# Performance work log

Hardware: AMD Instinct MI355X
Metric: run time of the kernel (lower is better)

Reference implementation:

```python
import jax, jax.numpy as jnp
import numpy as np

DIM = 512
N_HEADS = 8
HEAD_DIM = DIM // N_HEADS


def setup_inputs() -> dict:
    key = jax.random.key(0)
    ks = jax.random.split(key, 11)
    B, S = 2, 2048
    s = 1.0 / np.sqrt(DIM)
    return {
        "q": jax.random.normal(ks[0], (B, S, DIM), jnp.float32),
        "k": jax.random.normal(ks[1], (B, S, DIM), jnp.float32),
        "v": jax.random.normal(ks[2], (B, S, DIM), jnp.float32),
        "Wq": jax.random.normal(ks[3], (DIM, DIM), jnp.float32) * s,
        "bq": jnp.zeros((DIM,), jnp.float32),
        "Wk": jax.random.normal(ks[4], (DIM, DIM), jnp.float32) * s,
        "bk": jnp.zeros((DIM,), jnp.float32),
        "Wv": jax.random.normal(ks[5], (DIM, DIM), jnp.float32) * s,
        "bv": jnp.zeros((DIM,), jnp.float32),
        "Wo": jax.random.normal(ks[6], (DIM, DIM), jnp.float32) * s,
        "bo": jnp.zeros((DIM,), jnp.float32),
    }


def reference(q, k, v, Wq, bq, Wk, bk, Wv, bv, Wo, bo):
    B, S, _ = q.shape
    # projections; split into heads: [B, H, S, Dh]
    def proj(x, W, b):
        y = x @ W.T + b
        return y.reshape(B, -1, N_HEADS, HEAD_DIM).transpose(0, 2, 1, 3)

    qh = proj(q, Wq, bq)
    kh = proj(k, Wk, bk)
    vh = proj(v, Wv, bv)
    scores = jnp.einsum("bhsd,bhtd->bhst", qh, kh) / np.sqrt(HEAD_DIM)
    attn = jax.nn.softmax(scores, axis=-1)  # dropout = identity in eval
    ctx = jnp.einsum("bhst,bhtd->bhsd", attn, vh)
    ctx = ctx.transpose(0, 2, 1, 3).reshape(B, S, DIM)
    out = ctx @ Wo.T + bo
    return out, attn
```

## Files before the change

### kernel.cpp

```cpp
#include <hip/hip_runtime.h>
#include <math.h>

#define DIM 512
#define NH 8
#define HD 64
#define SS 2048
#define NB 2

typedef __bf16 bf16;
typedef __attribute__((ext_vector_type(8))) __bf16 bf16x8;
typedef __attribute__((ext_vector_type(4))) __bf16 bf16x4;
typedef __attribute__((ext_vector_type(2))) __bf16 bf16x2;
typedef __attribute__((ext_vector_type(4))) float f32x4;

__device__ inline bf16x8 cvt8(const float* s) {
  bf16x8 o;
#pragma unroll
  for (int i = 0; i < 8; ++i) o[i] = (bf16)s[i];
  return o;
}

__device__ inline void bar_lds_only() {
  asm volatile("s_waitcnt lgkmcnt(0)" ::: "memory");
  __builtin_amdgcn_s_barrier();
}

__global__ __launch_bounds__(256) void qkv_proj_kernel(
    const float* __restrict__ xq, const float* __restrict__ xk, const float* __restrict__ xv,
    const float* __restrict__ Wq, const float* __restrict__ bq,
    const float* __restrict__ Wk, const float* __restrict__ bk,
    const float* __restrict__ Wv, const float* __restrict__ bv,
    bf16* __restrict__ qh, bf16* __restrict__ kh, bf16* __restrict__ vh)
{
  const int which = blockIdx.z;
  const float* A    = (which == 0) ? xq : (which == 1) ? xk : xv;
  const float* W    = (which == 0) ? Wq : (which == 1) ? Wk : Wv;
  const float* bias = (which == 0) ? bq : (which == 1) ? bk : bv;
  bf16* out         = (which == 0) ? qh : (which == 1) ? kh : vh;
  const float oscale = (which == 0) ? 0.125f : 1.0f;

  __shared__ bf16 As[128][72];
  __shared__ bf16 Bs[64][72];

  const int m0 = blockIdx.x * 128;
  const int n0 = blockIdx.y * 64;
  const int tid = threadIdx.x;
  const int w = tid >> 6, l = tid & 63;
  const int l16 = l & 15, lg = l >> 4;
  const int wm = w >> 1, wn = w & 1;

  f32x4 acc[4][2];
#pragma unroll
  for (int mf = 0; mf < 4; ++mf)
#pragma unroll
    for (int nf = 0; nf < 2; ++nf) acc[mf][nf] = (f32x4){0.f, 0.f, 0.f, 0.f};

  for (int k0 = 0; k0 < DIM; k0 += 64) {
    __syncthreads();
    {
      const int r = tid >> 1, hf = (tid & 1) * 32;
      const float* src = &A[(size_t)(m0 + r) * DIM + k0 + hf];
      bf16* dst = &As[r][hf];
#pragma unroll
      for (int i = 0; i < 4; ++i) ((bf16x8*)dst)[i] = cvt8(src + i * 8);
    }
    if (tid < 128) {
      const int r = tid >> 1, hf = (tid & 1) * 32;
      const float* src = &W[(size_t)(n0 + r) * DIM + k0 + hf];
      bf16* dst = &Bs[r][hf];
#pragma unroll
      for (int i = 0; i < 4; ++i) ((bf16x8*)dst)[i] = cvt8(src + i * 8);
    }
    __syncthreads();

#pragma unroll
    for (int kk = 0; kk < 2; ++kk) {
      bf16x8 bfr[2];
      bfr[0] = *(const bf16x8*)&Bs[wn * 32 + l16][kk * 32 + lg * 8];
      bfr[1] = *(const bf16x8*)&Bs[wn * 32 + 16 + l16][kk * 32 + lg * 8];
#pragma unroll
      for (int mf = 0; mf < 4; ++mf) {
        const bf16x8 af = *(const bf16x8*)&As[wm * 64 + mf * 16 + l16][kk * 32 + lg * 8];
        acc[mf][0] = __builtin_amdgcn_mfma_f32_16x16x32_bf16(af, bfr[0], acc[mf][0], 0, 0, 0);
        acc[mf][1] = __builtin_amdgcn_mfma_f32_16x16x32_bf16(af, bfr[1], acc[mf][1], 0, 0, 0);
      }
    }
  }

  const int h = blockIdx.y;
#pragma unroll
  for (int mf = 0; mf < 4; ++mf) {
#pragma unroll
    for (int nf = 0; nf < 2; ++nf) {
      const int d = wn * 32 + nf * 16 + l16;
#pragma unroll
      for (int ri = 0; ri < 4; ++ri) {
        const int row = m0 + wm * 64 + mf * 16 + lg * 4 + ri;
        const int b = row >> 11, s = row & 2047;
        out[((size_t)(b * NH + h) * SS + s) * HD + d] =
            (bf16)((acc[mf][nf][ri] + bias[n0 + d]) * oscale);
      }
    }
  }
}

__global__ __launch_bounds__(512, 4) void attn_kernel(
    const bf16* __restrict__ qh, const bf16* __restrict__ kh, const bf16* __restrict__ vh,
    float* __restrict__ attn, bf16* __restrict__ ctx)
{
  __shared__ __align__(16) bf16 Ks[2][64][72];
  __shared__ __align__(16) bf16 Vt[2][64][72];
  __shared__ __align__(16) bf16 Ps[8][16][128];
  __shared__ float mlred[2][4][16];

  const int lin  = blockIdx.x;
  const int work = (lin & 7) * 64 + (lin >> 3);
  const int bh = work >> 5;
  const int q0 = (work & 31) * 64;

  const int tid = threadIdx.x;
  const int w   = tid >> 6;
  const int wq  = w >> 1;
  const int wt  = w & 1;
  const int l   = tid & 63;
  const int l16 = l & 15;
  const int lg  = l >> 4;

  const bf16* qp = qh + (size_t)bh * SS * HD;
  const bf16* kp = kh + (size_t)bh * SS * HD;
  const bf16* vp = vh + (size_t)bh * SS * HD;

  const int ks_wt = tid >> 8;
  const int ks_r  = (tid >> 2) & 63;
  const int ks_c  = (tid & 3) * 16;
  const int vs_wt = tid >> 8;
  const int vs_rc = (tid >> 3) & 31;
  const int vs_dc = tid & 7;

  const bf16* kstage = &kp[(size_t)(ks_wt * 1024 + ks_r) * HD + ks_c];
  const bf16* vstage = &vp[(size_t)(vs_wt * 1024 + vs_rc * 2) * HD + vs_dc * 8];
  bf16* ks_dst = &Ks[ks_wt][ks_r][ks_c];
  const int vcolbase = (((vs_rc >> 2) ^ vs_dc) << 3) | ((vs_rc & 3) << 1);

  const int qrow = q0 + wq * 16 + l16;
  const bf16x8 qf0 = *(const bf16x8*)&qp[(size_t)qrow * HD + lg * 8];
  const bf16x8 qf1 = *(const bf16x8*)&qp[(size_t)qrow * HD + 32 + lg * 8];

  const int tbase = wt * 1024;

  float lsum = 0.f;
  {
    const bf16* src = kstage;
    ((bf16x8*)ks_dst)[0] = ((const bf16x8*)src)[0];
    ((bf16x8*)ks_dst)[1] = ((const bf16x8*)src)[1];
  }
  for (int tt = 0; tt < 1024; tt += 64) {
    bf16x8 kr0, kr1;
    const bool has_next = (tt + 64) < 1024;
    if (has_next) {
      const bf16* src = kstage + (size_t)(tt + 64) * HD;
      kr0 = ((const bf16x8*)src)[0];
      kr1 = ((const bf16x8*)src)[1];
    }
    bar_lds_only();

#pragma unroll
    for (int n = 0; n < 4; ++n) {
      const bf16x8 kf0 = *(const bf16x8*)&Ks[wt][n * 16 + l16][lg * 8];
      const bf16x8 kf1 = *(const bf16x8*)&Ks[wt][n * 16 + l16][32 + lg * 8];
      f32x4 a = {0.f, 0.f, 0.f, 0.f};
      a = __builtin_amdgcn_mfma_f32_16x16x32_bf16(kf0, qf0, a, 0, 0, 0);
      a = __builtin_amdgcn_mfma_f32_16x16x32_bf16(kf1, qf1, a, 0, 0, 0);
#pragma unroll
      for (int reg = 0; reg < 4; ++reg) lsum += __expf(a[reg]);
    }
    bar_lds_only();
    if (has_next) {
      ((bf16x8*)ks_dst)[0] = kr0;
      ((bf16x8*)ks_dst)[1] = kr1;
    }
  }
  lsum += __shfl_xor(lsum, 16);
  lsum += __shfl_xor(lsum, 32);
  if (lg == 0) mlred[wt][wq][l16] = lsum;
  __syncthreads();
  const float inv_l = 1.f / (mlred[0][wq][l16] + mlred[1][wq][l16]);

  f32x4 accC[4];
#pragma unroll
  for (int dt = 0; dt < 4; ++dt) accC[dt] = (f32x4){0.f, 0.f, 0.f, 0.f};

  float* arow = attn + ((size_t)(bh * SS + q0 + wq * 16 + l16)) * SS + tbase;
  char* psbase = (char*)&Ps[w][0][0] + l16 * 256;

  {
    const bf16* src = kstage;
    ((bf16x8*)ks_dst)[0] = ((const bf16x8*)src)[0];
    ((bf16x8*)ks_dst)[1] = ((const bf16x8*)src)[1];
    const bf16x8 v0 = *(const bf16x8*)vstage;
    const bf16x8 v1 = *(const bf16x8*)(vstage + HD);
#pragma unroll
    for (int j = 0; j < 8; ++j) {
      *(bf16x2*)&Vt[vs_wt][vs_dc * 8 + j][vcolbase] = (bf16x2){v0[j], v1[j]};
    }
  }

  for (int tt = 0; tt < 1024; tt += 64) {
    bf16x8 kr0, kr1, vr0, vr1;
    const bool has_next = (tt + 64) < 1024;
    if (has_next) {
      const bf16* ksrc = kstage + (size_t)(tt + 64) * HD;
      kr0 = ((const bf16x8*)ksrc)[0];
      kr1 = ((const bf16x8*)ksrc)[1];
      const bf16* vsrc = vstage + (size_t)(tt + 64) * HD;
      vr0 = *(const bf16x8*)vsrc;
      vr1 = *(const bf16x8*)(vsrc + HD);
    }
    bar_lds_only();

#pragma unroll
    for (int n = 0; n < 4; ++n) {
      const bf16x8 kf0 = *(const bf16x8*)&Ks[wt][n * 16 + l16][lg * 8];
      const bf16x8 kf1 = *(const bf16x8*)&Ks[wt][n * 16 + l16][32 + lg * 8];
      f32x4 a = {0.f, 0.f, 0.f, 0.f};
      a = __builtin_amdgcn_mfma_f32_16x16x32_bf16(kf0, qf0, a, 0, 0, 0);
      a = __builtin_amdgcn_mfma_f32_16x16x32_bf16(kf1, qf1, a, 0, 0, 0);

      float4 pv;
      bf16x4 p4;
#pragma unroll
      for (int reg = 0; reg < 4; ++reg) {
        const float p = __expf(a[reg]) * inv_l;
        ((float*)&pv)[reg] = p;
        p4[reg] = (bf16)p;
      }
      *(float4*)&arow[tt + n * 16 + lg * 4] = pv;
      *(bf16x4*)(psbase + ((((n << 1) | (lg >> 1)) ^ (l16 & 7)) << 4) + ((lg & 1) << 3)) = p4;
    }

#pragma unroll
    for (int ts = 0; ts < 2; ++ts) {
      const bf16x8 pa = *(const bf16x8*)(psbase + ((((ts << 2) | lg) ^ (l16 & 7)) << 4));
#pragma unroll
      for (int dt = 0; dt < 4; ++dt) {
        const int vcol = (((ts * 4 + lg) ^ ((dt * 2 + (l16 >> 3)) & 7)) << 3);
        const bf16x8 vb = *(const bf16x8*)&Vt[wt][dt * 16 + l16][vcol];
        accC[dt] = __builtin_amdgcn_mfma_f32_16x16x32_bf16(vb, pa, accC[dt], 0, 0, 0);
      }
    }
    bar_lds_only();
    if (has_next) {
      ((bf16x8*)ks_dst)[0] = kr0;
      ((bf16x8*)ks_dst)[1] = kr1;
#pragma unroll
      for (int j = 0; j < 8; ++j) {
        *(bf16x2*)&Vt[vs_wt][vs_dc * 8 + j][vcolbase] = (bf16x2){vr0[j], vr1[j]};
      }
    }
  }

  __syncthreads();
  float* cred = (float*)&Ks[0][0][0];
  if (wt == 1) {
#pragma unroll
    for (int dt = 0; dt < 4; ++dt)
      *(f32x4*)&cred[(wq * 16 + l16) * 68 + dt * 16 + lg * 4] = accC[dt];
  }
  __syncthreads();
  if (wt == 0) {
    const int b = bh >> 3, h = bh & 7;
    bf16* crow = ctx + ((size_t)b * SS + q0 + wq * 16 + l16) * DIM + h * HD;
#pragma unroll
    for (int dt = 0; dt < 4; ++dt) {
      const f32x4 o = *(const f32x4*)&cred[(wq * 16 + l16) * 68 + dt * 16 + lg * 4];
      bf16x4 cb;
#pragma unroll
      for (int reg = 0; reg < 4; ++reg) cb[reg] = (bf16)(accC[dt][reg] + o[reg]);
      *(bf16x4*)&crow[dt * 16 + lg * 4] = cb;
    }
  }
}

__global__ __launch_bounds__(256) void out_proj_kernel(
    const bf16* __restrict__ ctx, const float* __restrict__ Wo, const float* __restrict__ bo,
    float* __restrict__ out)
{
  __shared__ bf16 As[128][72];
  __shared__ bf16 Bs[64][72];

  const int m0 = blockIdx.x * 128;
  const int n0 = blockIdx.y * 64;
  const int tid = threadIdx.x;
  const int w = tid >> 6, l = tid & 63;
  const int l16 = l & 15, lg = l >> 4;
  const int wm = w >> 1, wn = w & 1;

  f32x4 acc[4][2];
#pragma unroll
  for (int mf = 0; mf < 4; ++mf)
#pragma unroll
    for (int nf = 0; nf < 2; ++nf) acc[mf][nf] = (f32x4){0.f, 0.f, 0.f, 0.f};

  for (int k0 = 0; k0 < DIM; k0 += 64) {
    __syncthreads();
    {
      const int r = tid >> 1, hf = (tid & 1) * 32;
      const bf16* src = &ctx[(size_t)(m0 + r) * DIM + k0 + hf];
      bf16* dst = &As[r][hf];
#pragma unroll
      for (int i = 0; i < 4; ++i) ((bf16x8*)dst)[i] = ((const bf16x8*)src)[i];
    }
    if (tid < 128) {
      const int r = tid >> 1, hf = (tid & 1) * 32;
      const float* src = &Wo[(size_t)(n0 + r) * DIM + k0 + hf];
      bf16* dst = &Bs[r][hf];
#pragma unroll
      for (int i = 0; i < 4; ++i) ((bf16x8*)dst)[i] = cvt8(src + i * 8);
    }
    __syncthreads();

#pragma unroll
    for (int kk = 0; kk < 2; ++kk) {
      bf16x8 bfr[2];
      bfr[0] = *(const bf16x8*)&Bs[wn * 32 + l16][kk * 32 + lg * 8];
      bfr[1] = *(const bf16x8*)&Bs[wn * 32 + 16 + l16][kk * 32 + lg * 8];
#pragma unroll
      for (int mf = 0; mf < 4; ++mf) {
        const bf16x8 af = *(const bf16x8*)&As[wm * 64 + mf * 16 + l16][kk * 32 + lg * 8];
        acc[mf][0] = __builtin_amdgcn_mfma_f32_16x16x32_bf16(af, bfr[0], acc[mf][0], 0, 0, 0);
        acc[mf][1] = __builtin_amdgcn_mfma_f32_16x16x32_bf16(af, bfr[1], acc[mf][1], 0, 0, 0);
      }
    }
  }

#pragma unroll
  for (int mf = 0; mf < 4; ++mf) {
#pragma unroll
    for (int nf = 0; nf < 2; ++nf) {
      const int c = n0 + wn * 32 + nf * 16 + l16;
#pragma unroll
      for (int ri = 0; ri < 4; ++ri) {
        const int row = m0 + wm * 64 + mf * 16 + lg * 4 + ri;
        out[(size_t)row * DIM + c] = acc[mf][nf][ri] + bo[c];
      }
    }
  }
}

extern "C" void kernel_launch(void* const* d_in, const int* in_sizes, int n_in,
                              void* d_out, int out_size, void* d_ws, size_t ws_size,
                              hipStream_t stream) {
  const float* q  = (const float*)d_in[0];
  const float* k  = (const float*)d_in[1];
  const float* v  = (const float*)d_in[2];
  const float* Wq = (const float*)d_in[3];
  const float* bq = (const float*)d_in[4];
  const float* Wk = (const float*)d_in[5];
  const float* bk = (const float*)d_in[6];
  const float* Wv = (const float*)d_in[7];
  const float* bv = (const float*)d_in[8];
  const float* Wo = (const float*)d_in[9];
  const float* bo = (const float*)d_in[10];

  float* out0 = (float*)d_out;
  float* attn = out0 + (size_t)NB * SS * DIM;

  const size_t HSZ = (size_t)NB * NH * SS * HD;
  bf16* qh  = (bf16*)d_ws;
  bf16* kh  = qh + HSZ;
  bf16* vh  = kh + HSZ;
  bf16* ctx = vh + HSZ;

  dim3 g1(NB * SS / 128, DIM / 64, 3);
  qkv_proj_kernel<<<g1, 256, 0, stream>>>(q, k, v, Wq, bq, Wk, bk, Wv, bv, qh, kh, vh);

  dim3 g2(SS / 64 * NB * NH);
  attn_kernel<<<g2, 512, 0, stream>>>(qh, kh, vh, attn, ctx);

  dim3 g3(NB * SS / 128, DIM / 64);
  out_proj_kernel<<<g3, 256, 0, stream>>>(ctx, Wo, bo, out0);
}
```

Measured before the change: 140.2 us.

## Split softmax denominator pass into separate kernel with double-buffered K tiles

Moves the first pass (row sums of exp(QK^T)) out of the attention kernel into a dedicated sums_kernel. The new kernel uses 256-thread blocks, twice as many blocks, and a double-buffered K tile with one barrier per iteration. It writes per-half partial sums to workspace, which the attention kernel then reads instead of recomputing. This aims to raise occupancy and parallelism for the sum pass and to drop one barrier per tile. The cost is an extra kernel launch and a workspace round-trip, and the no-max exp softmax is kept as before.

```diff
diff --git a/kernel.cpp b/kernel.cpp
--- a/kernel.cpp
+++ b/kernel.cpp
@@ -104,14 +104,84 @@
   }
 }
 
+__global__ __launch_bounds__(256, 8) void sums_kernel(
+    const bf16* __restrict__ qh, const bf16* __restrict__ kh,
+    float* __restrict__ partial)
+{
+  __shared__ __align__(16) bf16 Ks[2][64][72];
+
+  const int lin  = blockIdx.x;
+  const int work = (lin & 7) * 128 + (lin >> 3);
+  const int half = work & 1;
+  const int qb   = (work >> 1) & 31;
+  const int bh   = work >> 6;
+  const int q0   = qb * 64;
+
+  const int tid = threadIdx.x;
+  const int w   = tid >> 6;
+  const int l   = tid & 63;
+  const int l16 = l & 15;
+  const int lg  = l >> 4;
+
+  const bf16* qp = qh + (size_t)bh * SS * HD;
+  const bf16* kp = kh + ((size_t)bh * SS + half * 1024) * HD;
+
+  const int ks_r = tid >> 2;
+  const int ks_c = (tid & 3) * 16;
+  const bf16* kstage = &kp[(size_t)ks_r * HD + ks_c];
+
+  const int qrow = q0 + w * 16 + l16;
+  const bf16x8 qf0 = *(const bf16x8*)&qp[(size_t)qrow * HD + lg * 8];
+  const bf16x8 qf1 = *(const bf16x8*)&qp[(size_t)qrow * HD + 32 + lg * 8];
+
+  {
+    ((bf16x8*)&Ks[0][ks_r][ks_c])[0] = ((const bf16x8*)kstage)[0];
+    ((bf16x8*)&Ks[0][ks_r][ks_c])[1] = ((const bf16x8*)kstage)[1];
+  }
+  bar_lds_only();
+
+  float lsum = 0.f;
+  int cur = 0;
+  for (int tt = 0; tt < 1024; tt += 64) {
+    bf16x8 kr0, kr1;
+    const bool has_next = (tt + 64) < 1024;
+    if (has_next) {
+      const bf16* src = kstage + (size_t)(tt + 64) * HD;
+      kr0 = ((const bf16x8*)src)[0];
+      kr1 = ((const bf16x8*)src)[1];
+    }
+
+#pragma unroll
+    for (int n = 0; n < 4; ++n) {
+      const bf16x8 kf0 = *(const bf16x8*)&Ks[cur][n * 16 + l16][lg * 8];
+      const bf16x8 kf1 = *(const bf16x8*)&Ks[cur][n * 16 + l16][32 + lg * 8];
+      f32x4 a = {0.f, 0.f, 0.f, 0.f};
+      a = __builtin_amdgcn_mfma_f32_16x16x32_bf16(kf0, qf0, a, 0, 0, 0);
+      a = __builtin_amdgcn_mfma_f32_16x16x32_bf16(kf1, qf1, a, 0, 0, 0);
+#pragma unroll
+      for (int reg = 0; reg < 4; ++reg) lsum += __expf(a[reg]);
+    }
+    if (has_next) {
+      ((bf16x8*)&Ks[cur ^ 1][ks_r][ks_c])[0] = kr0;
+      ((bf16x8*)&Ks[cur ^ 1][ks_r][ks_c])[1] = kr1;
+    }
+    bar_lds_only();
+    cur ^= 1;
+  }
+
+  lsum += __shfl_xor(lsum, 16);
+  lsum += __shfl_xor(lsum, 32);
+  if (lg == 0) partial[(((size_t)bh * SS) + q0 + w * 16 + l16) * 2 + half] = lsum;
+}
+
 __global__ __launch_bounds__(512, 4) void attn_kernel(
     const bf16* __restrict__ qh, const bf16* __restrict__ kh, const bf16* __restrict__ vh,
+    const float* __restrict__ partial,
     float* __restrict__ attn, bf16* __restrict__ ctx)
 {
   __shared__ __align__(16) bf16 Ks[2][64][72];
   __shared__ __align__(16) bf16 Vt[2][64][72];
   __shared__ __align__(16) bf16 Ps[8][16][128];
-  __shared__ float mlred[2][4][16];
 
   const int lin  = blockIdx.x;
   const int work = (lin & 7) * 64 + (lin >> 3);
@@ -148,43 +218,8 @@
 
   const int tbase = wt * 1024;
 
-  float lsum = 0.f;
-  {
-    const bf16* src = kstage;
-    ((bf16x8*)ks_dst)[0] = ((const bf16x8*)src)[0];
-    ((bf16x8*)ks_dst)[1] = ((const bf16x8*)src)[1];
-  }
-  for (int tt = 0; tt < 1024; tt += 64) {
-    bf16x8 kr0, kr1;
-    const bool has_next = (tt + 64) < 1024;
-    if (has_next) {
-      const bf16* src = kstage + (size_t)(tt + 64) * HD;
-      kr0 = ((const bf16x8*)src)[0];
-      kr1 = ((const bf16x8*)src)[1];
-    }
-    bar_lds_only();
-
-#pragma unroll
-    for (int n = 0; n < 4; ++n) {
-      const bf16x8 kf0 = *(const bf16x8*)&Ks[wt][n * 16 + l16][lg * 8];
-      const bf16x8 kf1 = *(const bf16x8*)&Ks[wt][n * 16 + l16][32 + lg * 8];
-      f32x4 a = {0.f, 0.f, 0.f, 0.f};
-      a = __builtin_amdgcn_mfma_f32_16x16x32_bf16(kf0, qf0, a, 0, 0, 0);
-      a = __builtin_amdgcn_mfma_f32_16x16x32_bf16(kf1, qf1, a, 0, 0, 0);
-#pragma unroll
-      for (int reg = 0; reg < 4; ++reg) lsum += __expf(a[reg]);
-    }
-    bar_lds_only();
-    if (has_next) {
-      ((bf16x8*)ks_dst)[0] = kr0;
-      ((bf16x8*)ks_dst)[1] = kr1;
-    }
-  }
-  lsum += __shfl_xor(lsum, 16);
-  lsum += __shfl_xor(lsum, 32);
-  if (lg == 0) mlred[wt][wq][l16] = lsum;
-  __syncthreads();
-  const float inv_l = 1.f / (mlred[0][wq][l16] + mlred[1][wq][l16]);
+  const float inv_l = 1.f / (partial[((size_t)bh * SS + qrow) * 2 + 0] +
+                             partial[((size_t)bh * SS + qrow) * 2 + 1]);
 
   f32x4 accC[4];
 #pragma unroll
@@ -194,9 +229,8 @@
   char* psbase = (char*)&Ps[w][0][0] + l16 * 256;
 
   {
-    const bf16* src = kstage;
-    ((bf16x8*)ks_dst)[0] = ((const bf16x8*)src)[0];
-    ((bf16x8*)ks_dst)[1] = ((const bf16x8*)src)[1];
+    ((bf16x8*)ks_dst)[0] = ((const bf16x8*)kstage)[0];
+    ((bf16x8*)ks_dst)[1] = ((const bf16x8*)kstage)[1];
     const bf16x8 v0 = *(const bf16x8*)vstage;
     const bf16x8 v1 = *(const bf16x8*)(vstage + HD);
 #pragma unroll
@@ -370,12 +404,16 @@
   bf16* kh  = qh + HSZ;
   bf16* vh  = kh + HSZ;
   bf16* ctx = vh + HSZ;
+  float* partial = (float*)(ctx + (size_t)NB * SS * DIM);
 
   dim3 g1(NB * SS / 128, DIM / 64, 3);
   qkv_proj_kernel<<<g1, 256, 0, stream>>>(q, k, v, Wq, bq, Wk, bk, Wv, bv, qh, kh, vh);
 
+  dim3 g2a(NB * NH * (SS / 64) * 2);
+  sums_kernel<<<g2a, 256, 0, stream>>>(qh, kh, partial);
+
   dim3 g2(SS / 64 * NB * NH);
-  attn_kernel<<<g2, 512, 0, stream>>>(qh, kh, vh, attn, ctx);
+  attn_kernel<<<g2, 512, 0, stream>>>(qh, kh, vh, partial, attn, ctx);
 
   dim3 g3(NB * SS / 128, DIM / 64);
   out_proj_kernel<<<g3, 256, 0, stream>>>(ctx, Wo, bo, out0);
```

New measurement: 139.5 us (median of 2 runs). About the same (-0.5%).
